# Kernel optimization log

Hardware: AMD Instinct MI355X
Metric: run time of the kernel (lower is better)

## Reference

```python
import jax, jax.numpy as jnp
import numpy as np

T, B, D, H = 64, 512, 768, 12
HD = D // H
EPS = 1e-8  # torch cosine_similarity eps


def setup_inputs() -> dict:
    key = jax.random.key(0)
    k0, k1, k2, k3 = jax.random.split(key, 4)
    node_embs = jax.random.normal(k0, (T, B, D), dtype=jnp.float32)
    in_proj_w = jax.random.normal(k1, (3 * D, D), dtype=jnp.float32) * 0.02
    in_proj_b = jnp.zeros((3 * D,), dtype=jnp.float32)
    out_proj_w = jax.random.normal(k2, (D, D), dtype=jnp.float32) * 0.02
    out_proj_b = jnp.zeros((D,), dtype=jnp.float32)
    return {"node_embs": node_embs, "in_proj_w": in_proj_w, "in_proj_b": in_proj_b,
            "out_proj_w": out_proj_w, "out_proj_b": out_proj_b}


def reference(node_embs, in_proj_w, in_proj_b, out_proj_w, out_proj_b):
    # node_embs: (T, B, D). Original loops over t calling MHA on (B, 1, D)
    # i.e. self-attention across the B axis with batch=1, fused here over T.
    qkv = jnp.einsum('tbd,ed->tbe', node_embs, in_proj_w) + in_proj_b  # (T, B, 3D)
    q, k, v = jnp.split(qkv, 3, axis=-1)

    def heads(x):  # (T, B, D) -> (T, H, B, HD)
        return x.reshape(T, B, H, HD).transpose(0, 2, 1, 3)

    q, k, v = heads(q), heads(k), heads(v)
    scores = jnp.einsum('thqd,thkd->thqk', q, k) / np.sqrt(HD).astype(np.float32)
    attn = jax.nn.softmax(scores, axis=-1)
    ctx = jnp.einsum('thqk,thkd->thqd', attn, v)  # (T, H, B, HD)
    ctx = ctx.transpose(0, 2, 1, 3).reshape(T, B, D)
    out = jnp.einsum('tbd,ed->tbe', ctx, out_proj_w) + out_proj_b  # (T, B, D)

    # cosine similarity between all pairs over B, then mean over first index
    norm = jnp.maximum(jnp.linalg.norm(out, axis=-1), EPS)  # (T, B)
    xn = out / norm[..., None]
    sim = jnp.einsum('tid,tjd->tij', xn, xn)  # (T, B, B)
    adj = sim.mean(axis=1)[..., None]  # (T, B, 1) == (T, B, N) with N=1
    return adj
```

## Files before the change

### kernel.cpp

```cpp
#include <hip/hip_runtime.h>

#define T_ 64
#define B_ 512
#define D_ 768
#define H_ 12
#define HD_ 64
#define M1 (T_*B_)
#define N_QKV (3*D_)

typedef __attribute__((ext_vector_type(8))) short short8;
typedef __attribute__((ext_vector_type(4))) float f32x4;

__device__ __forceinline__ unsigned short f2b(float f) {
  unsigned int u = __float_as_uint(f);
  u = (u + 0x7FFFu + ((u >> 16) & 1u)) >> 16;
  return (unsigned short)u;
}
__device__ __forceinline__ float b2f(unsigned short s) {
  return __uint_as_float(((unsigned int)s) << 16);
}

__device__ __forceinline__ void load_lds16(const unsigned short* g, unsigned short* l) {
  __builtin_amdgcn_global_load_lds(
      (const __attribute__((address_space(1))) unsigned int*)g,
      (__attribute__((address_space(3))) unsigned int*)l, 16, 0, 0);
}

#define N4_NODE 6291456
#define N4_WQKV 442368
#define N4_WOUT 147456
__global__ __launch_bounds__(256) void k_cast_all(
    const float* __restrict__ node, const float* __restrict__ wqkv,
    const float* __restrict__ wout, unsigned short* __restrict__ x_bf,
    unsigned short* __restrict__ wqkv_bf, unsigned short* __restrict__ wout_bf) {
  int i = blockIdx.x * 256 + threadIdx.x;
  const float* src; unsigned short* dst; int off;
  if (i < N4_NODE)                 { src = node; dst = x_bf;    off = i; }
  else if (i < N4_NODE + N4_WQKV)  { src = wqkv; dst = wqkv_bf; off = i - N4_NODE; }
  else                             { src = wout; dst = wout_bf; off = i - N4_NODE - N4_WQKV; }
  float4 v = ((const float4*)src)[off];
  ushort4 o;
  o.x = f2b(v.x); o.y = f2b(v.y); o.z = f2b(v.z); o.w = f2b(v.w);
  ((ushort4*)dst)[off] = o;
}

#define SB0() __builtin_amdgcn_sched_barrier(0)
#define BARF() do { SB0(); __builtin_amdgcn_s_barrier(); SB0(); } while (0)
#define WLG0() asm volatile("s_waitcnt lgkmcnt(0)" ::: "memory")
#define WVM6() asm volatile("s_waitcnt vmcnt(6)" ::: "memory")
#define WVM3() asm volatile("s_waitcnt vmcnt(3)" ::: "memory")
#define WVM0() asm volatile("s_waitcnt vmcnt(0)" ::: "memory")

#define STG(SLOT, GOFF) do { \
  load_lds16(Ag  + (GOFF), lds + (SLOT)*12288 + tid*8); \
  load_lds16(Bg0 + (GOFF), lds + (SLOT)*12288 + 4096 + tid*8); \
  load_lds16(Bg1 + (GOFF), lds + (SLOT)*12288 + 8192 + tid*8); \
} while (0)

#define RD(GU) do { \
  const unsigned short* ga_ = lds + (GU)*12288; \
  aF[0] = *(const short8*)(ga_ + aBase); \
  aF[1] = *(const short8*)(ga_ + aBase + 512); \
  aF[2] = *(const short8*)(ga_ + aBase + 1024); \
  aF[3] = *(const short8*)(ga_ + aBase + 1536); \
  bF[0] = *(const short8*)(ga_ + bBase); \
  bF[1] = *(const short8*)(ga_ + bBase + 512); \
  bF[2] = *(const short8*)(ga_ + bBase + 1024); \
  bF[3] = *(const short8*)(ga_ + bBase + 1536); \
} while (0)

#define MM() do { \
  __builtin_amdgcn_s_setprio(1); \
  _Pragma("unroll") \
  for (int mf = 0; mf < 4; mf++) \
    _Pragma("unroll") \
    for (int nf = 0; nf < 4; nf++) \
      acc[mf][nf] = __builtin_amdgcn_mfma_f32_16x16x32_bf16(aF[mf], bF[nf], acc[mf][nf], 0, 0, 0); \
  __builtin_amdgcn_s_setprio(0); \
} while (0)

#define PHASE(GU, GOFF) do { RD(GU); STG(((GU)+3)&3, GOFF); WVM6(); WLG0(); MM(); BARF(); } while (0)

#define GEMM_RING_KLOOP(Aptr, Bptr) \
  const int tid = threadIdx.x; \
  const int lane = tid & 63, wave = tid >> 6; \
  const int ln = lane & 15, quad = lane >> 4; \
  const int wm = wave & 1, wn = wave >> 1; \
   \
  const int w_ = tid & 7, g_ = tid >> 3; \
  const int rowS_ = ((g_ >> 2) << 3) + (w_ & 4) + (g_ & 3); \
  const int octS_ = (w_ & 3) ^ (g_ & 3); \
  const unsigned short* Ag = Aptr + (size_t)(m0 + rowS_)*768 + octS_*8; \
  const unsigned short* Bg0 = Bptr + (size_t)(n0 + rowS_)*768 + octS_*8; \
  const unsigned short* Bg1 = Bg0 + (size_t)128*768; \
   \
  const int ra_ = wm*64 + ln; \
  const int aBase = ((((ra_>>3)*4 + (ra_&3))*8) + ((ra_&7) ^ quad)) * 8; \
  const int rb_ = (wn & 1)*64 + ln; \
  const int bBase = 4096 + (wn>>1)*4096 + \
      ((((rb_>>3)*4 + (rb_&3))*8) + ((rb_&7) ^ quad)) * 8; \
  short8 aF[4], bF[4]; \
  f32x4 acc[4][4] = {}; \
  STG(0, 0); STG(1, 32); STG(2, 64); \
  WVM6(); BARF(); \
  for (int J = 0; J < 5; ++J) { \
    PHASE(0, 96); PHASE(1, 128); PHASE(2, 160); PHASE(3, 192); \
    Ag += 128; Bg0 += 128; Bg1 += 128; \
  } \
   \
  RD(0); STG(3, 96); WVM6(); WLG0(); MM(); BARF(); \
  RD(1); WVM3(); WLG0(); MM(); BARF(); \
  RD(2); WVM0(); WLG0(); MM(); BARF(); \
  RD(3); WLG0(); MM(); \
  __syncthreads();

__global__ __launch_bounds__(512, 2) void k_gemm_qkv8(
    const unsigned short* __restrict__ A,
    const unsigned short* __restrict__ Bw,
    const float* __restrict__ bias,
    unsigned short* __restrict__ qo,
    unsigned short* __restrict__ ko,
    unsigned short* __restrict__ vTo)
{
  extern __shared__ __align__(16) unsigned short lds[];
  const int bb = blockIdx.x;
  const int xcd = bb & 7, idx = bb >> 3;
  const int m0 = (xcd*32 + idx/9) * 128;
  const int n0 = (idx%9) * 256;
  GEMM_RING_KLOOP(A, Bw)

  const int t = m0 >> 9, mb = m0 & 511;
  if (n0 < 1536) {
#pragma unroll
    for (int nf = 0; nf < 4; nf++) {
      const int col = wn*64 + nf*16 + ln;
      const float bi = bias[n0 + col];
      const int cc = col >> 3, cs = col & 7;
#pragma unroll
      for (int mf = 0; mf < 4; mf++) {
        const int row = wm*64 + mf*16 + quad*4;
#pragma unroll
        for (int r = 0; r < 4; r++) {
          const int rw = row + r;
          lds[rw*256 + ((cc ^ (rw&7))<<3) + cs] = f2b(acc[mf][nf][r] + bi);
        }
      }
    }
    __syncthreads();
    unsigned short* dst = (n0 < 768) ? qo : ko;
    const int colbase = (n0 < 768) ? n0 : n0 - 768;
#pragma unroll
    for (int it = 0; it < 8; it++) {
      int ci = it*512 + tid;
      int r2 = ci >> 5, cj = ci & 31;
      int within = colbase + cj*8;
      int h = within >> 6, hd = within & 63;
      *(uint4*)&dst[((size_t)(t*H_ + h)*B_ + mb + r2)*HD_ + hd] =
          *(const uint4*)&lds[r2*256 + ((cj ^ (r2&7))<<3)];
    }
  } else {
#pragma unroll
    for (int nf = 0; nf < 4; nf++) {
      const int col = wn*64 + nf*16 + ln;
      const float bi = bias[n0 + col];
#pragma unroll
      for (int mf = 0; mf < 4; mf++) {
        const int row = wm*64 + mf*16 + quad*4;
        ushort4 pk;
        pk.x = f2b(acc[mf][nf][0] + bi);
        pk.y = f2b(acc[mf][nf][1] + bi);
        pk.z = f2b(acc[mf][nf][2] + bi);
        pk.w = f2b(acc[mf][nf][3] + bi);
        *(ushort4*)&lds[col*128 + (((row>>3) ^ (col&7))<<3) + (row&7)] = pk;
      }
    }
    __syncthreads();
#pragma unroll
    for (int it = 0; it < 8; it++) {
      int ci = it*512 + tid;
      int r2 = ci >> 4, cj = ci & 15;
      int cg = (n0 - 1536) + r2;
      int h = cg >> 6, hd = cg & 63;
      *(uint4*)&vTo[((size_t)(t*H_ + h)*HD_ + hd)*B_ + mb + cj*8] =
          *(const uint4*)&lds[r2*128 + ((cj ^ (r2&7))<<3)];
    }
  }
}

__global__ __launch_bounds__(512, 2) void k_gemm_out8(
    const unsigned short* __restrict__ A,
    const unsigned short* __restrict__ Bw,
    const float* __restrict__ bias,
    unsigned short* __restrict__ outb)
{
  extern __shared__ __align__(16) unsigned short lds[];
  const int bb = blockIdx.x;
  const int xcd = bb & 7, idx = bb >> 3;
  const int m0 = (xcd*32 + idx/3) * 128;
  const int n0 = (idx%3) * 256;
  GEMM_RING_KLOOP(A, Bw)

#pragma unroll
  for (int nf = 0; nf < 4; nf++) {
    const int col = wn*64 + nf*16 + ln;
    const float bi = bias[n0 + col];
    const int cc = col >> 3, cs = col & 7;
#pragma unroll
    for (int mf = 0; mf < 4; mf++) {
      const int row = wm*64 + mf*16 + quad*4;
#pragma unroll
      for (int r = 0; r < 4; r++) {
        const int rw = row + r;
        lds[rw*256 + ((cc ^ (rw&7))<<3) + cs] = f2b(acc[mf][nf][r] + bi);
      }
    }
  }
  __syncthreads();
#pragma unroll
  for (int it = 0; it < 8; it++) {
    int ci = it*512 + tid;
    int r2 = ci >> 5, cj = ci & 31;
    *(uint4*)&outb[(size_t)(m0 + r2)*768 + n0 + cj*8] =
        *(const uint4*)&lds[r2*256 + ((cj ^ (r2&7))<<3)];
  }
}

__global__ __launch_bounds__(512) void k_attn(
    const unsigned short* __restrict__ q,
    const unsigned short* __restrict__ k,
    const unsigned short* __restrict__ vT,
    unsigned short* __restrict__ ctx)
{
  __shared__ __align__(16) unsigned short Ks[64*64];
  __shared__ __align__(16) unsigned short VT[64*64];
  __shared__ __align__(16) unsigned short Ps[8*32*72];
  __shared__ float Dn[8*64];
  const int tid = threadIdx.x;
  const int lane = tid & 63, wave = tid >> 6;
  const int ln = lane & 15, quad = lane >> 4;
  const int pxr = 8 * (ln >> 2);
  const int bb = blockIdx.x;
  const int xcd = bb & 7, idx = bb >> 3;
  const int th = xcd*96 + (idx >> 1);
  const int q0 = (idx & 1) * 256;
  const int t = th / H_, h = th - t*H_;
  const size_t base  = (size_t)th * (B_*HD_);
  const size_t baseT = (size_t)th * (HD_*B_);

  short8 qf[2][2];
#pragma unroll
  for (int s = 0; s < 2; s++) {
    const unsigned short* qp = &q[base + (size_t)(q0 + wave*32 + s*16 + ln)*HD_ + quad*8];
    qf[s][0] = *(const short8*)qp;
    qf[s][1] = *(const short8*)(qp + 32);
  }
  f32x4 acc[2][4] = {};
  float dpart[2] = {0.f, 0.f};
  unsigned short* Pw = &Ps[wave*32*72];

  for (int kt = 0; kt < B_; kt += 64) {
    __syncthreads();
    {
      int s = tid;
      int r = s >> 3, cp = s & 7, c = cp ^ (r & 7);
      load_lds16(&k[base + (size_t)(kt + r)*HD_ + c*8], &Ks[s*8]);
      load_lds16(&vT[baseT + (size_t)r*B_ + kt + c*8], &VT[s*8]);
    }
    __syncthreads();
    f32x4 sf[2][4] = {};
#pragma unroll
    for (int ki = 0; ki < 4; ki++) {
      int row = ki*16 + ln;
      short8 kf0 = *(const short8*)&Ks[row*64 + (quad     ^ (row & 7))*8];
      short8 kf1 = *(const short8*)&Ks[row*64 + ((4+quad) ^ (row & 7))*8];
#pragma unroll
      for (int s = 0; s < 2; s++) {
        sf[s][ki] = __builtin_amdgcn_mfma_f32_16x16x32_bf16(kf0, qf[s][0], sf[s][ki], 0, 0, 0);
        sf[s][ki] = __builtin_amdgcn_mfma_f32_16x16x32_bf16(kf1, qf[s][1], sf[s][ki], 0, 0, 0);
      }
    }
#pragma unroll
    for (int s = 0; s < 2; s++)
#pragma unroll
      for (int ki = 0; ki < 4; ki++) {
        float p0 = __expf(sf[s][ki][0] * 0.125f);
        float p1 = __expf(sf[s][ki][1] * 0.125f);
        float p2 = __expf(sf[s][ki][2] * 0.125f);
        float p3 = __expf(sf[s][ki][3] * 0.125f);
        dpart[s] += (p0 + p1) + (p2 + p3);
        uint2 uu;
        uu.x = (__float_as_uint(p1) & 0xFFFF0000u) | (__float_as_uint(p0) >> 16);
        uu.y = (__float_as_uint(p3) & 0xFFFF0000u) | (__float_as_uint(p2) >> 16);
        int col = (ki*16 + quad*4) ^ pxr;
        *(uint2*)&Pw[(s*16 + ln)*72 + col] = uu;
      }
    short8 pa[2][2];
#pragma unroll
    for (int s = 0; s < 2; s++)
#pragma unroll
      for (int hf = 0; hf < 2; hf++)
        pa[s][hf] = *(const short8*)&Pw[(s*16 + ln)*72 + ((hf*32 + quad*8) ^ pxr)];
#pragma unroll
    for (int ds = 0; ds < 4; ds++) {
      int row = ds*16 + ln;
      short8 vb0 = *(const short8*)&VT[row*64 + (quad     ^ (row & 7))*8];
      short8 vb1 = *(const short8*)&VT[row*64 + ((4+quad) ^ (row & 7))*8];
#pragma unroll
      for (int s = 0; s < 2; s++) {
        acc[s][ds] = __builtin_amdgcn_mfma_f32_16x16x32_bf16(pa[s][0], vb0, acc[s][ds], 0, 0, 0);
        acc[s][ds] = __builtin_amdgcn_mfma_f32_16x16x32_bf16(pa[s][1], vb1, acc[s][ds], 0, 0, 0);
      }
    }
  }
#pragma unroll
  for (int s = 0; s < 2; s++) {
    float d = dpart[s];
    d += __shfl_xor(d, 16);
    d += __shfl_xor(d, 32);
    if (quad == 0) Dn[wave*64 + s*16 + ln] = d;
  }
#pragma unroll
  for (int s = 0; s < 2; s++) {
    int qrow = q0 + wave*32 + s*16 + quad*4;
#pragma unroll
    for (int r = 0; r < 4; r++) {
      float invd = 1.f / Dn[wave*64 + s*16 + quad*4 + r];
      size_t o = ((size_t)t*B_ + (qrow + r))*D_ + h*HD_ + ln;
#pragma unroll
      for (int ds = 0; ds < 4; ds++)
        ctx[o + ds*16] = f2b(acc[s][ds][r] * invd);
    }
  }
}

__global__ __launch_bounds__(256) void k_norms1(const unsigned short* __restrict__ outb,
                                                float* __restrict__ norms,
                                                float* __restrict__ pmvec)
{
  __shared__ float wsum[4*768];
  int blk = blockIdx.x;
  int t = blk >> 3, c = blk & 7;
  int wave = threadIdx.x >> 6, lane = threadIdx.x & 63;
  float macc[12];
#pragma unroll
  for (int j = 0; j < 12; j++) macc[j] = 0.f;
  for (int i = 0; i < 16; i++) {
    int b = c*64 + wave*16 + i;
    const unsigned short* row = &outb[((size_t)t*B_ + b)*D_];
    float x[12]; float ss = 0.f;
#pragma unroll
    for (int j = 0; j < 12; j++) { x[j] = b2f(row[lane + 64*j]); ss += x[j]*x[j]; }
#pragma unroll
    for (int off = 32; off; off >>= 1) ss += __shfl_xor(ss, off);
    float nr = fmaxf(sqrtf(ss), 1e-8f);
    if (lane == 0) norms[(size_t)t*B_ + b] = nr;
    float inv = 1.f / nr;
#pragma unroll
    for (int j = 0; j < 12; j++) macc[j] += x[j]*inv;
  }
#pragma unroll
  for (int j = 0; j < 12; j++) wsum[wave*768 + 64*j + lane] = macc[j];
  __syncthreads();
  for (int d = threadIdx.x; d < 768; d += 256) {
    pmvec[(size_t)blk*768 + d] = wsum[d] + wsum[768 + d] + wsum[1536 + d] + wsum[2304 + d];
  }
}

__global__ __launch_bounds__(256) void k_norms2(const float* __restrict__ pmvec,
                                                float* __restrict__ mvec)
{
  int t = blockIdx.x;
  for (int d = threadIdx.x; d < 768; d += 256) {
    float s = 0.f;
#pragma unroll
    for (int c = 0; c < 8; c++) s += pmvec[(size_t)(t*8 + c)*768 + d];
    mvec[t*768 + d] = s * (1.0f/512.0f);
  }
}

__global__ __launch_bounds__(256) void k_adj(const unsigned short* __restrict__ outb,
                                             const float* __restrict__ norms,
                                             const float* __restrict__ mvec,
                                             float* __restrict__ adj)
{
  int idx = blockIdx.x*4 + (threadIdx.x >> 6);
  int lane = threadIdx.x & 63;
  int t = idx >> 9;
  const unsigned short* row = &outb[(size_t)idx*768];
  const float* m = &mvec[t*768];
  float dot = 0.f;
#pragma unroll
  for (int j = 0; j < 12; j++) dot += b2f(row[lane + 64*j]) * m[lane + 64*j];
#pragma unroll
  for (int off = 32; off; off >>= 1) dot += __shfl_xor(dot, off);
  if (lane == 0) adj[idx] = dot / norms[idx];
}

extern "C" void kernel_launch(void* const* d_in, const int* in_sizes, int n_in,
                              void* d_out, int out_size, void* d_ws, size_t ws_size,
                              hipStream_t stream)
{
  const float* node = (const float*)d_in[0];
  const float* wqkv = (const float*)d_in[1];
  const float* bqkv = (const float*)d_in[2];
  const float* wout = (const float*)d_in[3];
  const float* bout = (const float*)d_in[4];
  float* adj = (float*)d_out;

  char* ws = (char*)d_ws;
  const size_t SZ = (size_t)M1*D_*2;
  unsigned short* q_bf    = (unsigned short*)(ws);
  unsigned short* k_bf    = (unsigned short*)(ws + SZ);
  unsigned short* vT_bf   = (unsigned short*)(ws + 2*SZ);
  unsigned short* ctx_bf  = (unsigned short*)(ws + 3*SZ);
  unsigned short* x_bf    = (unsigned short*)(ws + 4*SZ);
  unsigned short* wqkv_bf = (unsigned short*)(ws + 5*SZ);
  unsigned short* wout_bf = (unsigned short*)(ws + 5*SZ + 3538944);
  unsigned short* out_bf  = (unsigned short*)(ws);
  float* pmvec            = (float*)(ws + 4*SZ);
  float* norms            = (float*)(ws + 5*SZ + 3538944 + 1179648);
  float* mvec             = (float*)(ws + 5*SZ + 3538944 + 1179648 + 131072);

  static int shmem_set = 0;
  if (!shmem_set) {
    hipFuncSetAttribute((const void*)k_gemm_qkv8,
                        hipFuncAttributeMaxDynamicSharedMemorySize, 98304);
    hipFuncSetAttribute((const void*)k_gemm_out8,
                        hipFuncAttributeMaxDynamicSharedMemorySize, 98304);
    shmem_set = 1;
  }

  k_cast_all<<<26880, 256, 0, stream>>>(node, wqkv, wout, x_bf, wqkv_bf, wout_bf);
  k_gemm_qkv8<<<2304, 512, 98304, stream>>>(x_bf, wqkv_bf, bqkv, q_bf, k_bf, vT_bf);
  k_attn<<<1536, 512, 0, stream>>>(q_bf, k_bf, vT_bf, ctx_bf);
  k_gemm_out8<<<768, 512, 98304, stream>>>(ctx_bf, wout_bf, bout, out_bf);
  k_norms1<<<T_*8, 256, 0, stream>>>(out_bf, norms, pmvec);
  k_norms2<<<T_, 256, 0, stream>>>(pmvec, mvec);
  k_adj<<<M1/4, 256, 0, stream>>>(out_bf, norms, mvec, adj);
}
```

Measured before the change: 452.4 us.

## Enlarge GEMM tiles to 256x256 with three-stage LDS ring

```diff
diff --git a/kernel.cpp b/kernel.cpp
--- a/kernel.cpp
+++ b/kernel.cpp
@@ -47,39 +47,35 @@
 #define SB0() __builtin_amdgcn_sched_barrier(0)
 #define BARF() do { SB0(); __builtin_amdgcn_s_barrier(); SB0(); } while (0)
 #define WLG0() asm volatile("s_waitcnt lgkmcnt(0)" ::: "memory")
-#define WVM6() asm volatile("s_waitcnt vmcnt(6)" ::: "memory")
-#define WVM3() asm volatile("s_waitcnt vmcnt(3)" ::: "memory")
+#define WVM4() asm volatile("s_waitcnt vmcnt(4)" ::: "memory")
 #define WVM0() asm volatile("s_waitcnt vmcnt(0)" ::: "memory")
 
 #define STG(SLOT, GOFF) do { \
-  load_lds16(Ag  + (GOFF), lds + (SLOT)*12288 + tid*8); \
-  load_lds16(Bg0 + (GOFF), lds + (SLOT)*12288 + 4096 + tid*8); \
-  load_lds16(Bg1 + (GOFF), lds + (SLOT)*12288 + 8192 + tid*8); \
+  load_lds16(Ag  + (GOFF),          lds + (SLOT)*16384 + tid*8); \
+  load_lds16(Ag  + 98304 + (GOFF),  lds + (SLOT)*16384 + 4096 + tid*8); \
+  load_lds16(Bg0 + (GOFF),          lds + (SLOT)*16384 + 8192 + tid*8); \
+  load_lds16(Bg0 + 98304 + (GOFF),  lds + (SLOT)*16384 + 12288 + tid*8); \
 } while (0)
 
 #define RD(GU) do { \
-  const unsigned short* ga_ = lds + (GU)*12288; \
-  aF[0] = *(const short8*)(ga_ + aBase); \
-  aF[1] = *(const short8*)(ga_ + aBase + 512); \
-  aF[2] = *(const short8*)(ga_ + aBase + 1024); \
-  aF[3] = *(const short8*)(ga_ + aBase + 1536); \
-  bF[0] = *(const short8*)(ga_ + bBase); \
-  bF[1] = *(const short8*)(ga_ + bBase + 512); \
-  bF[2] = *(const short8*)(ga_ + bBase + 1024); \
-  bF[3] = *(const short8*)(ga_ + bBase + 1536); \
+  const unsigned short* ga_ = lds + (GU)*16384; \
+  _Pragma("unroll") \
+  for (int mf = 0; mf < 8; mf++) aF[mf] = *(const short8*)(ga_ + aBase + mf*512); \
+  _Pragma("unroll") \
+  for (int nf = 0; nf < 4; nf++) bF[nf] = *(const short8*)(ga_ + bBase + nf*512); \
 } while (0)
 
 #define MM() do { \
   __builtin_amdgcn_s_setprio(1); \
   _Pragma("unroll") \
-  for (int mf = 0; mf < 4; mf++) \
+  for (int mf = 0; mf < 8; mf++) \
     _Pragma("unroll") \
     for (int nf = 0; nf < 4; nf++) \
       acc[mf][nf] = __builtin_amdgcn_mfma_f32_16x16x32_bf16(aF[mf], bF[nf], acc[mf][nf], 0, 0, 0); \
   __builtin_amdgcn_s_setprio(0); \
 } while (0)
 
-#define PHASE(GU, GOFF) do { RD(GU); STG(((GU)+3)&3, GOFF); WVM6(); WLG0(); MM(); BARF(); } while (0)
+#define PHASE(GU, SSLOT, GOFF) do { RD(GU); STG(SSLOT, GOFF); WVM4(); WLG0(); MM(); BARF(); } while (0)
 
 #define GEMM_RING_KLOOP(Aptr, Bptr) \
   const int tid = threadIdx.x; \
@@ -92,26 +88,22 @@
   const int octS_ = (w_ & 3) ^ (g_ & 3); \
   const unsigned short* Ag = Aptr + (size_t)(m0 + rowS_)*768 + octS_*8; \
   const unsigned short* Bg0 = Bptr + (size_t)(n0 + rowS_)*768 + octS_*8; \
-  const unsigned short* Bg1 = Bg0 + (size_t)128*768; \
    \
-  const int ra_ = wm*64 + ln; \
-  const int aBase = ((((ra_>>3)*4 + (ra_&3))*8) + ((ra_&7) ^ quad)) * 8; \
-  const int rb_ = (wn & 1)*64 + ln; \
-  const int bBase = 4096 + (wn>>1)*4096 + \
-      ((((rb_>>3)*4 + (rb_&3))*8) + ((rb_&7) ^ quad)) * 8; \
-  short8 aF[4], bF[4]; \
-  f32x4 acc[4][4] = {}; \
-  STG(0, 0); STG(1, 32); STG(2, 64); \
-  WVM6(); BARF(); \
-  for (int J = 0; J < 5; ++J) { \
-    PHASE(0, 96); PHASE(1, 128); PHASE(2, 160); PHASE(3, 192); \
-    Ag += 128; Bg0 += 128; Bg1 += 128; \
+  const int inner_ = (((ln>>3)*4 + (ln&3))*8 + ((ln&7) ^ quad)) * 8; \
+  const int aBase = wm*4096 + inner_; \
+  const int bBase = 8192 + (wn>>1)*4096 + (wn&1)*2048 + inner_; \
+  short8 aF[8], bF[4]; \
+  f32x4 acc[8][4] = {}; \
+  STG(0, 0); STG(1, 32); \
+  WVM4(); BARF(); \
+  for (int J = 0; J < 7; ++J) { \
+    PHASE(0, 2, 64); PHASE(1, 0, 96); PHASE(2, 1, 128); \
+    Ag += 96; Bg0 += 96; \
   } \
    \
-  RD(0); STG(3, 96); WVM6(); WLG0(); MM(); BARF(); \
-  RD(1); WVM3(); WLG0(); MM(); BARF(); \
-  RD(2); WVM0(); WLG0(); MM(); BARF(); \
-  RD(3); WLG0(); MM(); \
+  RD(0); STG(2, 64); WVM4(); WLG0(); MM(); BARF(); \
+  RD(1); WVM0(); WLG0(); MM(); BARF(); \
+  RD(2); WLG0(); MM(); \
   __syncthreads();
 
 __global__ __launch_bounds__(512, 2) void k_gemm_qkv8(
@@ -125,64 +117,77 @@
   extern __shared__ __align__(16) unsigned short lds[];
   const int bb = blockIdx.x;
   const int xcd = bb & 7, idx = bb >> 3;
-  const int m0 = (xcd*32 + idx/9) * 128;
+  const int m0 = (xcd*16 + idx/9) * 256;
   const int n0 = (idx%9) * 256;
   GEMM_RING_KLOOP(A, Bw)
 
   const int t = m0 >> 9, mb = m0 & 511;
   if (n0 < 1536) {
-#pragma unroll
-    for (int nf = 0; nf < 4; nf++) {
-      const int col = wn*64 + nf*16 + ln;
-      const float bi = bias[n0 + col];
-      const int cc = col >> 3, cs = col & 7;
-#pragma unroll
-      for (int mf = 0; mf < 4; mf++) {
-        const int row = wm*64 + mf*16 + quad*4;
-#pragma unroll
-        for (int r = 0; r < 4; r++) {
-          const int rw = row + r;
-          lds[rw*256 + ((cc ^ (rw&7))<<3) + cs] = f2b(acc[mf][nf][r] + bi);
-        }
-      }
-    }
-    __syncthreads();
     unsigned short* dst = (n0 < 768) ? qo : ko;
     const int colbase = (n0 < 768) ? n0 : n0 - 768;
 #pragma unroll
-    for (int it = 0; it < 8; it++) {
-      int ci = it*512 + tid;
-      int r2 = ci >> 5, cj = ci & 31;
-      int within = colbase + cj*8;
-      int h = within >> 6, hd = within & 63;
-      *(uint4*)&dst[((size_t)(t*H_ + h)*B_ + mb + r2)*HD_ + hd] =
-          *(const uint4*)&lds[r2*256 + ((cj ^ (r2&7))<<3)];
+    for (int half = 0; half < 2; half++) {
+      __syncthreads();
+      if (wm == half) {
+#pragma unroll
+        for (int nf = 0; nf < 4; nf++) {
+          const int col = wn*64 + nf*16 + ln;
+          const float bi = bias[n0 + col];
+          const int cc = col >> 3, cs = col & 7;
+#pragma unroll
+          for (int mf = 0; mf < 8; mf++) {
+            const int row = mf*16 + quad*4;
+#pragma unroll
+            for (int r = 0; r < 4; r++) {
+              const int rw = row + r;
+              lds[rw*256 + ((cc ^ (rw&7))<<3) + cs] = f2b(acc[mf][nf][r] + bi);
+            }
+          }
+        }
+      }
+      __syncthreads();
+#pragma unroll
+      for (int it = 0; it < 8; it++) {
+        int ci = it*512 + tid;
+        int r2 = ci >> 5, cj = ci & 31;
+        int within = colbase + cj*8;
+        int h = within >> 6, hd = within & 63;
+        *(uint4*)&dst[((size_t)(t*H_ + h)*B_ + mb + half*128 + r2)*HD_ + hd] =
+            *(const uint4*)&lds[r2*256 + ((cj ^ (r2&7))<<3)];
+      }
     }
   } else {
 #pragma unroll
-    for (int nf = 0; nf < 4; nf++) {
-      const int col = wn*64 + nf*16 + ln;
-      const float bi = bias[n0 + col];
-#pragma unroll
-      for (int mf = 0; mf < 4; mf++) {
-        const int row = wm*64 + mf*16 + quad*4;
-        ushort4 pk;
-        pk.x = f2b(acc[mf][nf][0] + bi);
-        pk.y = f2b(acc[mf][nf][1] + bi);
-        pk.z = f2b(acc[mf][nf][2] + bi);
-        pk.w = f2b(acc[mf][nf][3] + bi);
-        *(ushort4*)&lds[col*128 + (((row>>3) ^ (col&7))<<3) + (row&7)] = pk;
-      }
-    }
-    __syncthreads();
-#pragma unroll
-    for (int it = 0; it < 8; it++) {
-      int ci = it*512 + tid;
-      int r2 = ci >> 4, cj = ci & 15;
-      int cg = (n0 - 1536) + r2;
-      int h = cg >> 6, hd = cg & 63;
-      *(uint4*)&vTo[((size_t)(t*H_ + h)*HD_ + hd)*B_ + mb + cj*8] =
-          *(const uint4*)&lds[r2*128 + ((cj ^ (r2&7))<<3)];
+    for (int ch = 0; ch < 2; ch++) {
+      __syncthreads();
+      if ((wn >> 1) == ch) {
+#pragma unroll
+        for (int nf = 0; nf < 4; nf++) {
+          const int col = wn*64 + nf*16 + ln;
+          const int cl = col & 127;
+          const float bi = bias[n0 + col];
+#pragma unroll
+          for (int mf = 0; mf < 8; mf++) {
+            const int row = wm*128 + mf*16 + quad*4;
+            ushort4 pk;
+            pk.x = f2b(acc[mf][nf][0] + bi);
+            pk.y = f2b(acc[mf][nf][1] + bi);
+            pk.z = f2b(acc[mf][nf][2] + bi);
+            pk.w = f2b(acc[mf][nf][3] + bi);
+            *(ushort4*)&lds[cl*256 + (((row>>3) ^ (cl&7))<<3) + (row&7)] = pk;
+          }
+        }
+      }
+      __syncthreads();
+#pragma unroll
+      for (int it = 0; it < 8; it++) {
+        int ci = it*512 + tid;
+        int r2 = ci >> 5, cj = ci & 31;
+        int cg = (n0 - 1536) + ch*128 + r2;
+        int h = cg >> 6, hd = cg & 63;
+        *(uint4*)&vTo[((size_t)(t*H_ + h)*HD_ + hd)*B_ + mb + cj*8] =
+            *(const uint4*)&lds[r2*256 + ((cj ^ (r2&7))<<3)];
+      }
     }
   }
 }
@@ -196,32 +201,38 @@
   extern __shared__ __align__(16) unsigned short lds[];
   const int bb = blockIdx.x;
   const int xcd = bb & 7, idx = bb >> 3;
-  const int m0 = (xcd*32 + idx/3) * 128;
+  const int m0 = (xcd*16 + idx/3) * 256;
   const int n0 = (idx%3) * 256;
   GEMM_RING_KLOOP(A, Bw)
 
 #pragma unroll
-  for (int nf = 0; nf < 4; nf++) {
-    const int col = wn*64 + nf*16 + ln;
-    const float bi = bias[n0 + col];
-    const int cc = col >> 3, cs = col & 7;
-#pragma unroll
-    for (int mf = 0; mf < 4; mf++) {
-      const int row = wm*64 + mf*16 + quad*4;
-#pragma unroll
-      for (int r = 0; r < 4; r++) {
-        const int rw = row + r;
-        lds[rw*256 + ((cc ^ (rw&7))<<3) + cs] = f2b(acc[mf][nf][r] + bi);
-      }
-    }
-  }
-  __syncthreads();
-#pragma unroll
-  for (int it = 0; it < 8; it++) {
-    int ci = it*512 + tid;
-    int r2 = ci >> 5, cj = ci & 31;
-    *(uint4*)&outb[(size_t)(m0 + r2)*768 + n0 + cj*8] =
-        *(const uint4*)&lds[r2*256 + ((cj ^ (r2&7))<<3)];
+  for (int half = 0; half < 2; half++) {
+    __syncthreads();
+    if (wm == half) {
+#pragma unroll
+      for (int nf = 0; nf < 4; nf++) {
+        const int col = wn*64 + nf*16 + ln;
+        const float bi = bias[n0 + col];
+        const int cc = col >> 3, cs = col & 7;
+#pragma unroll
+        for (int mf = 0; mf < 8; mf++) {
+          const int row = mf*16 + quad*4;
+#pragma unroll
+          for (int r = 0; r < 4; r++) {
+            const int rw = row + r;
+            lds[rw*256 + ((cc ^ (rw&7))<<3) + cs] = f2b(acc[mf][nf][r] + bi);
+          }
+        }
+      }
+    }
+    __syncthreads();
+#pragma unroll
+    for (int it = 0; it < 8; it++) {
+      int ci = it*512 + tid;
+      int r2 = ci >> 5, cj = ci & 31;
+      *(uint4*)&outb[(size_t)(m0 + half*128 + r2)*768 + n0 + cj*8] =
+          *(const uint4*)&lds[r2*256 + ((cj ^ (r2&7))<<3)];
+    }
   }
 }
 
@@ -431,9 +442,9 @@
   }
 
   k_cast_all<<<26880, 256, 0, stream>>>(node, wqkv, wout, x_bf, wqkv_bf, wout_bf);
-  k_gemm_qkv8<<<2304, 512, 98304, stream>>>(x_bf, wqkv_bf, bqkv, q_bf, k_bf, vT_bf);
+  k_gemm_qkv8<<<1152, 512, 98304, stream>>>(x_bf, wqkv_bf, bqkv, q_bf, k_bf, vT_bf);
   k_attn<<<1536, 512, 0, stream>>>(q_bf, k_bf, vT_bf, ctx_bf);
-  k_gemm_out8<<<768, 512, 98304, stream>>>(ctx_bf, wout_bf, bout, out_bf);
+  k_gemm_out8<<<384, 512, 98304, stream>>>(ctx_bf, wout_bf, bout, out_bf);
   k_norms1<<<T_*8, 256, 0, stream>>>(out_bf, norms, pmvec);
   k_norms2<<<T_, 256, 0, stream>>>(pmvec, mvec);
   k_adj<<<M1/4, 256, 0, stream>>>(out_bf, norms, mvec, adj);
```

Measured after the change: 452.0 us. About the same (-0.1%).
